# Performance work log

Hardware: AMD Instinct MI355X
Metric: run time of the kernel (lower is better)

The kernel has to match this reference:

```python
import jax, jax.numpy as jnp
import numpy as np

DIM = 256
HEADS = 8
DIM_HEAD = 64
INNER = HEADS * DIM_HEAD  # 512
B, H, W = 4, 128, 128


def setup_inputs() -> dict:
    key = jax.random.key(0)
    ks = jax.random.split(key, 7)
    x = jax.random.normal(ks[0], (B, DIM, H, W), dtype=jnp.float32)
    context = jax.random.normal(ks[1], (B, DIM, H, W), dtype=jnp.float32)
    # weights stored as (in, out) so projection is x @ W
    s_in = 1.0 / np.sqrt(DIM)
    s_inner = 1.0 / np.sqrt(INNER)
    Wq = jax.random.uniform(ks[2], (DIM, INNER), jnp.float32, -s_in, s_in)
    Wk = jax.random.uniform(ks[3], (DIM, INNER), jnp.float32, -s_in, s_in)
    Wv = jax.random.uniform(ks[4], (DIM, INNER), jnp.float32, -s_in, s_in)
    Wo = jax.random.uniform(ks[5], (INNER, DIM), jnp.float32, -s_inner, s_inner)
    bo = jax.random.uniform(ks[6], (DIM,), jnp.float32, -s_inner, s_inner)
    return {"x": x, "context": context, "Wq": Wq, "Wk": Wk, "Wv": Wv, "Wo": Wo, "bo": bo}


def reference(x, context, Wq, Wk, Wv, Wo, bo):
    b, c, h, w = x.shape
    n = h * w
    x_flat = x.reshape(b, c, n).transpose(0, 2, 1)          # b n c
    ctx_flat = context.reshape(b, c, n).transpose(0, 2, 1)  # b n c
    # projections; split heads: b n (h d) -> b h n d
    def heads(t):
        return t.reshape(b, n, HEADS, DIM_HEAD).transpose(0, 2, 1, 3)
    q = heads(x_flat @ Wq)
    k = heads(ctx_flat @ Wk)
    v = heads(ctx_flat @ Wv)
    # column-wise softmax over token dim n (axis=-2). NOTE: original module
    # defines scale but never applies it, so we faithfully omit it.
    k = jax.nn.softmax(k, axis=-2)
    cm = jnp.einsum('bhnd,bhne->bhde', k, v)   # small d x e context matrix
    out = jnp.einsum('bhnd,bhde->bhne', q, cm)  # b h n e
    out = out.transpose(0, 2, 1, 3).reshape(b, n, INNER)
    out = out @ Wo + bo
    out = out.transpose(0, 2, 1).reshape(b, c, h, w)
    return x + out
```

## Files before the change

kernel.cpp:

```cpp
#include <hip/hip_runtime.h>

typedef unsigned short u16;
typedef u16   u16x4  __attribute__((ext_vector_type(4)));
typedef u16   u16x8  __attribute__((ext_vector_type(8)));
typedef __bf16 bf16x8 __attribute__((ext_vector_type(8)));
typedef float f32x4  __attribute__((ext_vector_type(4)));

constexpr int BATCH  = 4;
constexpr int CDIM   = 256;
constexpr int NTOK   = 16384;
constexpr int INNERD = 512;

__device__ __forceinline__ u16 f2b(float f) {
  return __builtin_bit_cast(u16, (__bf16)f);
}
__device__ __forceinline__ float b2f(u16 b) {
  return (float)__builtin_bit_cast(__bf16, b);
}

__device__ __forceinline__ void async_ld16(const u16* g, u16* l) {
  __builtin_amdgcn_global_load_lds(
      (const __attribute__((address_space(1))) void*)g,
      (__attribute__((address_space(3))) void*)l, 16, 0, 0);
}

constexpr int ZERO_N = BATCH * 8 * 64 * 64 + BATCH * INNERD;
__global__ __launch_bounds__(256) void prep(
    const float* __restrict__ x, const float* __restrict__ ctx,
    const float* __restrict__ Wk, const float* __restrict__ Wv,
    const float* __restrict__ Wq,
    u16* __restrict__ xt, u16* __restrict__ ct,
    u16* __restrict__ kt, u16* __restrict__ vt, u16* __restrict__ qc,
    float* __restrict__ zbuf) {
  __shared__ float tile[64][65];
  int id = blockIdx.x;
  int tid = threadIdx.x;
  if (id < 8192) {
    int bx = id & 255, by = (id >> 8) & 3, zb = id >> 10;
    int b = zb >> 1;
    const float* src = (zb & 1) ? ctx : x;
    u16* dst = (zb & 1) ? ct : xt;
    src += (size_t)b * CDIM * NTOK;
    dst += (size_t)b * NTOK * CDIM;
    int n0 = bx * 64, c0 = by * 64;
    int tx = tid & 15, ty = tid >> 4;
#pragma unroll
    for (int i = 0; i < 64; i += 16) {
      f32x4 v = *(const f32x4*)&src[(size_t)(c0 + ty + i) * NTOK + n0 + tx * 4];
#pragma unroll
      for (int j = 0; j < 4; j++) tile[ty + i][tx * 4 + j] = v[j];
    }
    __syncthreads();
    int nl = tid >> 3;
    int cl = (tid & 7) * 8;
#pragma unroll
    for (int j2 = 0; j2 < 2; j2++) {
      int nn = nl + 32 * j2;
      u16x8 o;
#pragma unroll
      for (int j = 0; j < 8; j++) o[j] = f2b(tile[cl + j][nn]);
      *(u16x8*)&dst[(size_t)(n0 + nn) * CDIM + c0 + cl] = o;
    }
  } else if (id < 8448) {
    int idw = id - 8192;
    int bx = idw & 15, by = (idw >> 4) & 7, bz = idw >> 7;
    float (*t2)[33] = (float(*)[33])tile;
    const float* src = bz == 0 ? Wk : Wv;
    u16* dst = bz == 0 ? kt : vt;
    int i0 = bx * 32, c0 = by * 32;
    int tx = tid & 31, ty = tid >> 5;
#pragma unroll
    for (int r = 0; r < 32; r += 8)
      t2[ty + r][tx] = src[(size_t)(c0 + ty + r) * INNERD + i0 + tx];
    __syncthreads();
#pragma unroll
    for (int r = 0; r < 32; r += 8)
      dst[(size_t)(i0 + ty + r) * CDIM + c0 + tx] = f2b(t2[tx][ty + r]);
  } else if (id < 8512) {
    size_t off = (size_t)(id - 8448) * 2048 + tid * 8;
    f32x4 a = *(const f32x4*)&Wq[off];
    f32x4 c = *(const f32x4*)&Wq[off + 4];
    u16x8 o;
#pragma unroll
    for (int j = 0; j < 4; j++) { o[j] = f2b(a[j]); o[j + 4] = f2b(c[j]); }
    *(u16x8*)&qc[off] = o;
  } else {
    int i = (id - 8512) * 256 + tid;
    if (i < ZERO_N) zbuf[i] = 0.0f;
  }
}

__global__ __launch_bounds__(256, 2) void proj_ctx(
    const u16* __restrict__ Wkt, const u16* __restrict__ Wvt,
    const u16* __restrict__ ctx_bt, float* __restrict__ cm, float* __restrict__ ksum) {
  int id = blockIdx.x;
  int swz = (id & 7) * 64 + (id >> 3);
  int ig = swz & 3, nc = (swz >> 2) & 31, b = swz >> 7;
  int i0 = ig * 128;
  const u16* Bt = ctx_bt + (size_t)b * NTOK * CDIM;

  __shared__ __align__(16) u16 smem[32768];
  u16* Ek = smem + 16384;
  u16* Vt = smem;

  int tid = threadIdx.x, wave = tid >> 6, lane = tid & 63;
  int wm = (wave >> 1) * 64, wn = (wave & 1) * 64;
  int quad = lane >> 4, l16 = lane & 15;
  int sr = lane >> 2, sc = (lane & 3) * 8;

  int hl = wave >> 1, dblk = (wave & 1) * 32;

  u16x8 ov;
#pragma unroll
  for (int t = 0; t < 8; t++) ov[t] = 0x3f80;
  const bf16x8 ones = __builtin_bit_cast(bf16x8, ov);

  f32x4 acc_cm[2][4];
  f32x4 accS[2];
#pragma unroll
  for (int i = 0; i < 2; i++) {
    accS[i] = (f32x4)(0.0f);
#pragma unroll
    for (int j = 0; j < 4; j++) acc_cm[i][j] = (f32x4)(0.0f);
  }

  auto stage = [&](int p, int kv, int ks, int n0) {
    int k0 = ks * 32;
    const u16* Asrc = kv ? Wvt : Wkt;
#pragma unroll
    for (int j = 0; j < 4; j++) {
      int c = wave * 4 + j;
      if (c < 8) {
        int row = c * 16 + sr;
        async_ld16(&Asrc[(size_t)(i0 + row) * CDIM + k0 + sc], &smem[p * 8192 + c * 512]);
      } else {
        int cb = c - 8, row = cb * 16 + sr;
        async_ld16(&Bt[(size_t)(n0 + row) * CDIM + k0 + sc], &smem[p * 8192 + 4096 + cb * 512]);
      }
    }
  };

  for (int nt = 0; nt < 4; nt++) {
    int n0 = nc * 512 + nt * 128;
    __syncthreads();
    stage(0, 0, 0, n0);
    __syncthreads();

    f32x4 acc[4][4];
#pragma unroll
    for (int i = 0; i < 4; i++)
#pragma unroll
      for (int j = 0; j < 4; j++) acc[i][j] = (f32x4)(0.0f);

#pragma unroll 2
    for (int s = 0; s < 16; s++) {
      int p = s & 1;
      if (s < 15) { int s1 = s + 1; stage(p ^ 1, s1 >> 3, s1 & 7, n0); }
      const u16* As = &smem[p * 8192];
      const u16* Bs = &smem[p * 8192 + 4096];
      bf16x8 af[4], bfr[4];
#pragma unroll
      for (int m = 0; m < 4; m++)
        af[m] = __builtin_bit_cast(bf16x8, *(const u16x8*)&As[(wm + m * 16 + l16) * 32 + quad * 8]);
#pragma unroll
      for (int e = 0; e < 4; e++)
        bfr[e] = __builtin_bit_cast(bf16x8, *(const u16x8*)&Bs[(wn + e * 16 + l16) * 32 + quad * 8]);
#pragma unroll
      for (int e = 0; e < 4; e++)
#pragma unroll
        for (int m = 0; m < 4; m++)
          acc[e][m] = __builtin_amdgcn_mfma_f32_16x16x32_bf16(bfr[e], af[m], acc[e][m], 0, 0, 0);

      if (s == 7) {
#pragma unroll
        for (int e = 0; e < 4; e++) {
          int nl0 = wn + e * 16 + quad * 4;
#pragma unroll
          for (int m = 0; m < 4; m++) {
            int row = wm + m * 16 + l16;
            u16x4 ok;
#pragma unroll
            for (int r = 0; r < 4; r++) ok[r] = f2b(__expf(acc[e][m][r]));
            unsigned byt = (unsigned)(row * 256 + nl0 * 2) ^ ((unsigned)(row & 7) << 4);
            *(u16x4*)((char*)Ek + byt) = ok;
            acc[e][m] = (f32x4)(0.0f);
          }
        }
      }
      __syncthreads();
    }
#pragma unroll
    for (int e = 0; e < 4; e++) {
      int nl0 = wn + e * 16 + quad * 4;
#pragma unroll
      for (int m = 0; m < 4; m++) {
        int row = wm + m * 16 + l16;
        u16x4 ovv;
#pragma unroll
        for (int r = 0; r < 4; r++) ovv[r] = f2b(acc[e][m][r]);
        unsigned byt = (unsigned)(row * 256 + nl0 * 2) ^ ((unsigned)(row & 7) << 4);
        *(u16x4*)((char*)Vt + byt) = ovv;
      }
    }
    __syncthreads();
#pragma unroll
    for (int kk = 0; kk < 128; kk += 32) {
      int ko = kk + quad * 8;
      bf16x8 ea[2], vb[4];
#pragma unroll
      for (int m2 = 0; m2 < 2; m2++) {
        int row = hl * 64 + dblk + m2 * 16 + l16;
        unsigned byt = (unsigned)(row * 256 + ko * 2) ^ ((unsigned)(row & 7) << 4);
        ea[m2] = __builtin_bit_cast(bf16x8, *(const u16x8*)((char*)Ek + byt));
      }
#pragma unroll
      for (int e2 = 0; e2 < 4; e2++) {
        int row = hl * 64 + e2 * 16 + l16;
        unsigned byt = (unsigned)(row * 256 + ko * 2) ^ ((unsigned)(row & 7) << 4);
        vb[e2] = __builtin_bit_cast(bf16x8, *(const u16x8*)((char*)Vt + byt));
      }
#pragma unroll
      for (int m2 = 0; m2 < 2; m2++) {
        accS[m2] = __builtin_amdgcn_mfma_f32_16x16x32_bf16(ea[m2], ones, accS[m2], 0, 0, 0);
#pragma unroll
        for (int e2 = 0; e2 < 4; e2++)
          acc_cm[m2][e2] = __builtin_amdgcn_mfma_f32_16x16x32_bf16(ea[m2], vb[e2], acc_cm[m2][e2], 0, 0, 0);
      }
    }
  }
  int h = ig * 2 + hl;
  float* cmp = cm + (size_t)(b * 8 + h) * 64 * 64;
#pragma unroll
  for (int m2 = 0; m2 < 2; m2++)
#pragma unroll
    for (int e2 = 0; e2 < 4; e2++)
#pragma unroll
      for (int r = 0; r < 4; r++) {
        int d = dblk + m2 * 16 + quad * 4 + r;
        int e = e2 * 16 + l16;
        atomicAdd(&cmp[d * 64 + e], acc_cm[m2][e2][r]);
      }
  if (l16 == 0) {
#pragma unroll
    for (int m2 = 0; m2 < 2; m2++)
#pragma unroll
      for (int r = 0; r < 4; r++) {
        int d = dblk + m2 * 16 + quad * 4 + r;
        atomicAdd(&ksum[(size_t)b * INNERD + h * 64 + d], accS[m2][r]);
      }
  }
}

__global__ __launch_bounds__(256) void weff_k(
    const float* __restrict__ cm, const float* __restrict__ Wo,
    const float* __restrict__ ksum, u16* __restrict__ weff_t) {
  int bi = blockIdx.x;
  int b = bi >> 9, i = bi & 511, h = i >> 6, d = i & 63;
  const float* cmr = cm + ((size_t)(b * 8 + h) * 64 + d) * 64;
  __shared__ float cs[64];
  if (threadIdx.x < 64) cs[threadIdx.x] = cmr[threadIdx.x];
  __syncthreads();
  float inv = 1.0f / ksum[(size_t)b * INNERD + i];
  int c = threadIdx.x;
  float s = 0.0f;
#pragma unroll 8
  for (int e = 0; e < 64; e++) s += cs[e] * Wo[(size_t)(h * 64 + e) * CDIM + c];
  weff_t[((size_t)b * CDIM + c) * INNERD + i] = f2b(s * inv);
}

__global__ __launch_bounds__(256) void gt_k(
    const u16* __restrict__ weff_t, const u16* __restrict__ Wqc, u16* __restrict__ Gt) {
  int id = blockIdx.x;
  int bx = id & 1, by = (id >> 1) & 1, b = id >> 2;
  const u16* A  = weff_t + (size_t)b * CDIM * INNERD;
  const u16* Bt = Wqc;
  int i0 = bx * 128;
  int n0 = by * 128;

  __shared__ __align__(16) u16 smem3[16384];

  int tid = threadIdx.x;
  int wave = tid >> 6, lane = tid & 63;
  int wm = (wave >> 1) * 64, wn = (wave & 1) * 64;
  int quad = lane >> 4, l16 = lane & 15;
  int sr = lane >> 2, sc = (lane & 3) * 8;

  auto stage = [&](int p, int ks) {
    int k0 = ks * 32;
#pragma unroll
    for (int j = 0; j < 4; j++) {
      int c = wave * 4 + j;
      if (c < 8) {
        int row = c * 16 + sr;
        async_ld16(&A[(size_t)(i0 + row) * INNERD + k0 + sc], &smem3[p * 8192 + c * 512]);
      } else {
        int cb = c - 8, row = cb * 16 + sr;
        async_ld16(&Bt[(size_t)(n0 + row) * INNERD + k0 + sc], &smem3[p * 8192 + 4096 + cb * 512]);
      }
    }
  };

  f32x4 acc[4][4];
#pragma unroll
  for (int i = 0; i < 4; i++)
#pragma unroll
    for (int j = 0; j < 4; j++) acc[i][j] = (f32x4)(0.0f);

  stage(0, 0);
  __syncthreads();
#pragma unroll 2
  for (int s = 0; s < 16; s++) {
    int p = s & 1;
    if (s < 15) stage(p ^ 1, s + 1);
    const u16* As = &smem3[p * 8192];
    const u16* Bs = &smem3[p * 8192 + 4096];
    bf16x8 af[4], bfr[4];
#pragma unroll
    for (int m = 0; m < 4; m++)
      af[m] = __builtin_bit_cast(bf16x8, *(const u16x8*)&As[(wm + m * 16 + l16) * 32 + quad * 8]);
#pragma unroll
    for (int e = 0; e < 4; e++)
      bfr[e] = __builtin_bit_cast(bf16x8, *(const u16x8*)&Bs[(wn + e * 16 + l16) * 32 + quad * 8]);
#pragma unroll
    for (int e = 0; e < 4; e++)
#pragma unroll
      for (int m = 0; m < 4; m++)
        acc[e][m] = __builtin_amdgcn_mfma_f32_16x16x32_bf16(bfr[e], af[m], acc[e][m], 0, 0, 0);
    if (s < 15) __syncthreads();
  }
#pragma unroll
  for (int e = 0; e < 4; e++) {
    int nb = n0 + wn + e * 16 + quad * 4;
#pragma unroll
    for (int m = 0; m < 4; m++) {
      int c = i0 + wm + m * 16 + l16;
      u16x4 o;
#pragma unroll
      for (int r = 0; r < 4; r++) o[r] = f2b(acc[e][m][r]);
      *(u16x4*)&Gt[((size_t)b * CDIM + c) * CDIM + nb] = o;
    }
  }
}

__global__ __launch_bounds__(256) void final_gemm(
    const u16* __restrict__ Gt, const u16* __restrict__ x_bt,
    const float* __restrict__ x, const float* __restrict__ bo,
    float* __restrict__ out) {
  int id = blockIdx.x;
  int swz = (id & 7) * 128 + (id >> 3);
  int bx = swz & 1, by = (swz >> 1) & 127, b = swz >> 8;
  const u16* A  = Gt + (size_t)b * CDIM * CDIM;
  const u16* Bt = x_bt + (size_t)b * NTOK * CDIM;
  const float* xb = x + (size_t)b * CDIM * NTOK;
  float* ob = out + (size_t)b * CDIM * NTOK;
  int i0 = bx * 128;
  int n0 = by * 128;

  __shared__ __align__(16) u16 smem2[16384];

  int tid = threadIdx.x;
  int wave = tid >> 6, lane = tid & 63;
  int wm = (wave >> 1) * 64, wn = (wave & 1) * 64;
  int quad = lane >> 4, l16 = lane & 15;
  int sr = lane >> 2, sc = (lane & 3) * 8;

  auto stage = [&](int p, int ks) {
    int k0 = ks * 32;
#pragma unroll
    for (int j = 0; j < 4; j++) {
      int c = wave * 4 + j;
      if (c < 8) {
        int row = c * 16 + sr;
        async_ld16(&A[(size_t)(i0 + row) * CDIM + k0 + sc], &smem2[p * 8192 + c * 512]);
      } else {
        int cb = c - 8, row = cb * 16 + sr;
        async_ld16(&Bt[(size_t)(n0 + row) * CDIM + k0 + sc], &smem2[p * 8192 + 4096 + cb * 512]);
      }
    }
  };

  f32x4 acc[4][4];
#pragma unroll
  for (int i = 0; i < 4; i++)
#pragma unroll
    for (int j = 0; j < 4; j++) acc[i][j] = (f32x4)(0.0f);

  stage(0, 0);
  __syncthreads();
#pragma unroll 2
  for (int s = 0; s < 8; s++) {
    int p = s & 1;
    if (s < 7) stage(p ^ 1, s + 1);
    const u16* As = &smem2[p * 8192];
    const u16* Bs = &smem2[p * 8192 + 4096];
    bf16x8 af[4], bfr[4];
#pragma unroll
    for (int m = 0; m < 4; m++)
      af[m] = __builtin_bit_cast(bf16x8, *(const u16x8*)&As[(wm + m * 16 + l16) * 32 + quad * 8]);
#pragma unroll
    for (int e = 0; e < 4; e++)
      bfr[e] = __builtin_bit_cast(bf16x8, *(const u16x8*)&Bs[(wn + e * 16 + l16) * 32 + quad * 8]);
#pragma unroll
    for (int e = 0; e < 4; e++)
#pragma unroll
      for (int m = 0; m < 4; m++)
        acc[e][m] = __builtin_amdgcn_mfma_f32_16x16x32_bf16(bfr[e], af[m], acc[e][m], 0, 0, 0);
    if (s < 7) __syncthreads();
  }
#pragma unroll
  for (int e = 0; e < 4; e++) {
    int nb = n0 + wn + e * 16 + quad * 4;
#pragma unroll
    for (int m = 0; m < 4; m++) {
      int c = i0 + wm + m * 16 + l16;
      f32x4 xv = *(const f32x4*)&xb[(size_t)c * NTOK + nb];
      f32x4 r;
      float bc = bo[c];
#pragma unroll
      for (int t = 0; t < 4; t++) r[t] = acc[e][m][t] + xv[t] + bc;
      *(f32x4*)&ob[(size_t)c * NTOK + nb] = r;
    }
  }
}

extern "C" void kernel_launch(void* const* d_in, const int* in_sizes, int n_in,
                              void* d_out, int out_size, void* d_ws, size_t ws_size,
                              hipStream_t stream) {
  const float* x   = (const float*)d_in[0];
  const float* ctx = (const float*)d_in[1];
  const float* Wq  = (const float*)d_in[2];
  const float* Wk  = (const float*)d_in[3];
  const float* Wv  = (const float*)d_in[4];
  const float* Wo  = (const float*)d_in[5];
  const float* bo  = (const float*)d_in[6];
  float* out = (float*)d_out;

  char* ws = (char*)d_ws;
  u16* ctx_bt = (u16*)ws;  ws += (size_t)BATCH * NTOK * CDIM * 2;
  u16* x_bt   = (u16*)ws;  ws += (size_t)BATCH * NTOK * CDIM * 2;
  u16* Wk_t   = (u16*)ws;  ws += (size_t)INNERD * CDIM * 2;
  u16* Wv_t   = (u16*)ws;  ws += (size_t)INNERD * CDIM * 2;
  u16* Wqc    = (u16*)ws;  ws += (size_t)CDIM * INNERD * 2;
  float* cm   = (float*)ws; ws += (size_t)BATCH * 8 * 64 * 64 * 4;
  float* ksum = (float*)ws; ws += (size_t)BATCH * INNERD * 4;
  u16* weff_t = (u16*)ws;  ws += (size_t)BATCH * CDIM * INNERD * 2;
  u16* Gt     = (u16*)ws;  ws += (size_t)BATCH * CDIM * CDIM * 2;

  prep<<<dim3(9032), 256, 0, stream>>>(x, ctx, Wk, Wv, Wq, x_bt, ctx_bt,
                                       Wk_t, Wv_t, Wqc, cm );
  proj_ctx<<<dim3(512), 256, 0, stream>>>(Wk_t, Wv_t, ctx_bt, cm, ksum);
  weff_k<<<BATCH * INNERD, 256, 0, stream>>>(cm, Wo, ksum, weff_t);
  gt_k<<<dim3(16), 256, 0, stream>>>(weff_t, Wqc, Gt);
  final_gemm<<<dim3(1024), 256, 0, stream>>>(Gt, x_bt, x, bo, out);
}
```

Before: 295.1 us.

## Double proj_ctx block to 512 threads with 8 waves splitting the tile

Launches proj_ctx with 8 waves per block instead of 4. Each wave now computes a 64x32 sub-tile of the projection and a 16-row slice of the context matrix, which halves per-wave accumulators and async loads. The aim is more latency hiding per CU and lower register pressure. Launch bounds change to (512,4), which may cap registers. LDS use per block stays at 64KB, so residency is likely limited by LDS rather than waves.

```diff
diff --git a/kernel.cpp b/kernel.cpp
--- a/kernel.cpp
+++ b/kernel.cpp
@@ -90,7 +90,7 @@
   }
 }
 
-__global__ __launch_bounds__(256, 2) void proj_ctx(
+__global__ __launch_bounds__(512, 4) void proj_ctx(
     const u16* __restrict__ Wkt, const u16* __restrict__ Wvt,
     const u16* __restrict__ ctx_bt, float* __restrict__ cm, float* __restrict__ ksum) {
   int id = blockIdx.x;
@@ -104,32 +104,28 @@
   u16* Vt = smem;
 
   int tid = threadIdx.x, wave = tid >> 6, lane = tid & 63;
-  int wm = (wave >> 1) * 64, wn = (wave & 1) * 64;
+  int wm = (wave >> 2) * 64, wn = (wave & 3) * 32;
   int quad = lane >> 4, l16 = lane & 15;
   int sr = lane >> 2, sc = (lane & 3) * 8;
 
-  int hl = wave >> 1, dblk = (wave & 1) * 32;
+  int hl = wave >> 2, dblk = (wave & 3) * 16;
 
   u16x8 ov;
 #pragma unroll
   for (int t = 0; t < 8; t++) ov[t] = 0x3f80;
   const bf16x8 ones = __builtin_bit_cast(bf16x8, ov);
 
-  f32x4 acc_cm[2][4];
-  f32x4 accS[2];
-#pragma unroll
-  for (int i = 0; i < 2; i++) {
-    accS[i] = (f32x4)(0.0f);
-#pragma unroll
-    for (int j = 0; j < 4; j++) acc_cm[i][j] = (f32x4)(0.0f);
-  }
+  f32x4 acc_cm[4];
+  f32x4 accS = (f32x4)(0.0f);
+#pragma unroll
+  for (int j = 0; j < 4; j++) acc_cm[j] = (f32x4)(0.0f);
 
   auto stage = [&](int p, int kv, int ks, int n0) {
     int k0 = ks * 32;
     const u16* Asrc = kv ? Wvt : Wkt;
 #pragma unroll
-    for (int j = 0; j < 4; j++) {
-      int c = wave * 4 + j;
+    for (int j = 0; j < 2; j++) {
+      int c = wave * 2 + j;
       if (c < 8) {
         int row = c * 16 + sr;
         async_ld16(&Asrc[(size_t)(i0 + row) * CDIM + k0 + sc], &smem[p * 8192 + c * 512]);
@@ -146,9 +142,9 @@
     stage(0, 0, 0, n0);
     __syncthreads();
 
-    f32x4 acc[4][4];
-#pragma unroll
-    for (int i = 0; i < 4; i++)
+    f32x4 acc[2][4];
+#pragma unroll
+    for (int i = 0; i < 2; i++)
 #pragma unroll
       for (int j = 0; j < 4; j++) acc[i][j] = (f32x4)(0.0f);
 
@@ -158,22 +154,22 @@
       if (s < 15) { int s1 = s + 1; stage(p ^ 1, s1 >> 3, s1 & 7, n0); }
       const u16* As = &smem[p * 8192];
       const u16* Bs = &smem[p * 8192 + 4096];
-      bf16x8 af[4], bfr[4];
+      bf16x8 af[4], bfr[2];
 #pragma unroll
       for (int m = 0; m < 4; m++)
         af[m] = __builtin_bit_cast(bf16x8, *(const u16x8*)&As[(wm + m * 16 + l16) * 32 + quad * 8]);
 #pragma unroll
-      for (int e = 0; e < 4; e++)
+      for (int e = 0; e < 2; e++)
         bfr[e] = __builtin_bit_cast(bf16x8, *(const u16x8*)&Bs[(wn + e * 16 + l16) * 32 + quad * 8]);
 #pragma unroll
-      for (int e = 0; e < 4; e++)
+      for (int e = 0; e < 2; e++)
 #pragma unroll
         for (int m = 0; m < 4; m++)
           acc[e][m] = __builtin_amdgcn_mfma_f32_16x16x32_bf16(bfr[e], af[m], acc[e][m], 0, 0, 0);
 
       if (s == 7) {
 #pragma unroll
-        for (int e = 0; e < 4; e++) {
+        for (int e = 0; e < 2; e++) {
           int nl0 = wn + e * 16 + quad * 4;
 #pragma unroll
           for (int m = 0; m < 4; m++) {
@@ -190,7 +186,7 @@
       __syncthreads();
     }
 #pragma unroll
-    for (int e = 0; e < 4; e++) {
+    for (int e = 0; e < 2; e++) {
       int nl0 = wn + e * 16 + quad * 4;
 #pragma unroll
       for (int m = 0; m < 4; m++) {
@@ -206,12 +202,11 @@
 #pragma unroll
     for (int kk = 0; kk < 128; kk += 32) {
       int ko = kk + quad * 8;
-      bf16x8 ea[2], vb[4];
-#pragma unroll
-      for (int m2 = 0; m2 < 2; m2++) {
-        int row = hl * 64 + dblk + m2 * 16 + l16;
+      bf16x8 ea, vb[4];
+      {
+        int row = hl * 64 + dblk + l16;
         unsigned byt = (unsigned)(row * 256 + ko * 2) ^ ((unsigned)(row & 7) << 4);
-        ea[m2] = __builtin_bit_cast(bf16x8, *(const u16x8*)((char*)Ek + byt));
+        ea = __builtin_bit_cast(bf16x8, *(const u16x8*)((char*)Ek + byt));
       }
 #pragma unroll
       for (int e2 = 0; e2 < 4; e2++) {
@@ -219,35 +214,28 @@
         unsigned byt = (unsigned)(row * 256 + ko * 2) ^ ((unsigned)(row & 7) << 4);
         vb[e2] = __builtin_bit_cast(bf16x8, *(const u16x8*)((char*)Vt + byt));
       }
-#pragma unroll
-      for (int m2 = 0; m2 < 2; m2++) {
-        accS[m2] = __builtin_amdgcn_mfma_f32_16x16x32_bf16(ea[m2], ones, accS[m2], 0, 0, 0);
-#pragma unroll
-        for (int e2 = 0; e2 < 4; e2++)
-          acc_cm[m2][e2] = __builtin_amdgcn_mfma_f32_16x16x32_bf16(ea[m2], vb[e2], acc_cm[m2][e2], 0, 0, 0);
-      }
+      accS = __builtin_amdgcn_mfma_f32_16x16x32_bf16(ea, ones, accS, 0, 0, 0);
+#pragma unroll
+      for (int e2 = 0; e2 < 4; e2++)
+        acc_cm[e2] = __builtin_amdgcn_mfma_f32_16x16x32_bf16(ea, vb[e2], acc_cm[e2], 0, 0, 0);
     }
   }
   int h = ig * 2 + hl;
   float* cmp = cm + (size_t)(b * 8 + h) * 64 * 64;
 #pragma unroll
-  for (int m2 = 0; m2 < 2; m2++)
-#pragma unroll
-    for (int e2 = 0; e2 < 4; e2++)
-#pragma unroll
-      for (int r = 0; r < 4; r++) {
-        int d = dblk + m2 * 16 + quad * 4 + r;
-        int e = e2 * 16 + l16;
-        atomicAdd(&cmp[d * 64 + e], acc_cm[m2][e2][r]);
-      }
+  for (int e2 = 0; e2 < 4; e2++)
+#pragma unroll
+    for (int r = 0; r < 4; r++) {
+      int d = dblk + quad * 4 + r;
+      int e = e2 * 16 + l16;
+      atomicAdd(&cmp[d * 64 + e], acc_cm[e2][r]);
+    }
   if (l16 == 0) {
 #pragma unroll
-    for (int m2 = 0; m2 < 2; m2++)
-#pragma unroll
-      for (int r = 0; r < 4; r++) {
-        int d = dblk + m2 * 16 + quad * 4 + r;
-        atomicAdd(&ksum[(size_t)b * INNERD + h * 64 + d], accS[m2][r]);
-      }
+    for (int r = 0; r < 4; r++) {
+      int d = dblk + quad * 4 + r;
+      atomicAdd(&ksum[(size_t)b * INNERD + h * 64 + d], accS[r]);
+    }
   }
 }
 
@@ -448,7 +436,7 @@
 
   prep<<<dim3(9032), 256, 0, stream>>>(x, ctx, Wk, Wv, Wq, x_bt, ctx_bt,
                                        Wk_t, Wv_t, Wqc, cm );
-  proj_ctx<<<dim3(512), 256, 0, stream>>>(Wk_t, Wv_t, ctx_bt, cm, ksum);
+  proj_ctx<<<dim3(512), 512, 0, stream>>>(Wk_t, Wv_t, ctx_bt, cm, ksum);
   weff_k<<<BATCH * INNERD, 256, 0, stream>>>(cm, Wo, ksum, weff_t);
   gt_k<<<dim3(16), 256, 0, stream>>>(weff_t, Wqc, Gt);
   final_gemm<<<dim3(1024), 256, 0, stream>>>(Gt, x_bt, x, bo, out);
```

Result: no change. 297.2 us (+0.7%).
